# Kernel optimization log

Hardware: AMD Instinct MI355X
Metric: run time of the kernel (lower is better)

The kernel has to match this reference:

```python
import jax, jax.numpy as jnp
import numpy as np

D_MODEL, H, D_FF = 512, 8, 2048
DK = D_MODEL // H
EPS = 1e-5  # torch LayerNorm default


def layer_norm(x, g, b):
    m = jnp.mean(x, axis=-1, keepdims=True)
    v = jnp.mean((x - m) ** 2, axis=-1, keepdims=True)
    return (x - m) * jax.lax.rsqrt(v + EPS) * g + b


def setup_inputs() -> dict:
    key = jax.random.key(0)
    ks = jax.random.split(key, 10)
    B, S = 8, 2048
    s = lambda fan_in: 1.0 / np.sqrt(fan_in)
    return {
        "x": jax.random.normal(ks[0], (B, S, D_MODEL), jnp.float32),
        # per-head projections stacked: [h, d_model, dk] (bias-free Project)
        "wq": jax.random.uniform(ks[1], (H, D_MODEL, DK), jnp.float32, -s(D_MODEL), s(D_MODEL)),
        "wk": jax.random.uniform(ks[2], (H, D_MODEL, DK), jnp.float32, -s(D_MODEL), s(D_MODEL)),
        "wv": jax.random.uniform(ks[3], (H, D_MODEL, DK), jnp.float32, -s(D_MODEL), s(D_MODEL)),
        "wo": jax.random.uniform(ks[4], (D_MODEL, D_MODEL), jnp.float32, -s(D_MODEL), s(D_MODEL)),
        "w1": jax.random.uniform(ks[5], (D_MODEL, D_FF), jnp.float32, -s(D_MODEL), s(D_MODEL)),
        "b1": jax.random.uniform(ks[6], (D_FF,), jnp.float32, -s(D_MODEL), s(D_MODEL)),
        "w2": jax.random.uniform(ks[7], (D_FF, D_MODEL), jnp.float32, -s(D_FF), s(D_FF)),
        "b2": jax.random.uniform(ks[8], (D_MODEL,), jnp.float32, -s(D_FF), s(D_FF)),
        "ln1_g": jnp.ones((D_MODEL,), jnp.float32),
        "ln1_b": jnp.zeros((D_MODEL,), jnp.float32),
        "ln2_g": jnp.ones((D_MODEL,), jnp.float32),
        "ln2_b": jnp.zeros((D_MODEL,), jnp.float32),
    }


def reference(x, wq, wk, wv, wo, w1, b1, w2, b2, ln1_g, ln1_b, ln2_g, ln2_b):
    B, S, D = x.shape
    # --- multi-head self-attention (8 per-head Linears fused into one einsum) ---
    q = jnp.einsum("bsd,hdk->bhsk", x, wq)
    k = jnp.einsum("bsd,hdk->bhsk", x, wk)
    v = jnp.einsum("bsd,hdk->bhsk", x, wv)
    score = jnp.einsum("bhsk,bhtk->bhst", q, k) * (1.0 / np.sqrt(DK))
    attn = jax.nn.softmax(score, axis=-1)
    heads = jnp.einsum("bhst,bhtk->bhsk", attn, v)
    concat = heads.transpose(0, 2, 1, 3).reshape(B, S, D)  # cat over heads
    mha = concat @ wo
    # dropout in eval mode -> identity
    x = layer_norm(mha + x, ln1_g, ln1_b)
    # --- feed-forward ---
    ffn = jax.nn.relu(x @ w1 + b1) @ w2 + b2
    return layer_norm(ffn + x, ln2_g, ln2_b)
```

## Files before the change

### kernel.cpp

```cpp
#include <hip/hip_runtime.h>
#include <hip/hip_bf16.h>
#include <math.h>


#define D_MODEL 512
#define NHEAD   8
#define DKH     64
#define SEQ     2048
#define BATCH   8
#define DFF     2048
#define MROWS   (BATCH * SEQ)
#define QKVLD   1536

typedef __bf16 bf16x8 __attribute__((ext_vector_type(8)));
typedef float  f32x4  __attribute__((ext_vector_type(4)));

__device__ __forceinline__ unsigned short f2bf(float f) {
    union { float f; unsigned u; } v; v.f = f;
    return (unsigned short)((v.u + 0x7FFFu + ((v.u >> 16) & 1u)) >> 16);
}

__device__ __forceinline__ float fexp2(float x) {
    float r; asm("v_exp_f32 %0, %1" : "=v"(r) : "v"(x)); return r;
}

__device__ __forceinline__ f32x4 mfma16(bf16x8 a, bf16x8 b, f32x4 c) {
    return __builtin_amdgcn_mfma_f32_16x16x32_bf16(a, b, c, 0, 0, 0);
}

template<bool BIAS, bool RELU, bool RES, bool OUTF32>
__global__ __launch_bounds__(256)
void mfma_gemm(const unsigned short* __restrict__ Av,
               const unsigned short* __restrict__ Bt,
               const float* __restrict__ bias, const float* __restrict__ res,
               void* __restrict__ Cv, int Kdim, int lda, int ldc)
{
    __shared__ unsigned short As[128][40];
    __shared__ unsigned short Bs[128][40];

    const int tid  = threadIdx.x;
    const int lane = tid & 63;
    const int w    = tid >> 6;
    const int mq   = (w >> 1) << 6;
    const int nq   = (w & 1) << 6;
    const int lrow = lane & 15;
    const int g    = lane >> 4;
    const int lk   = g << 3;

    const int row0 = blockIdx.y << 7;
    const int col0 = blockIdx.x << 7;

    const int sr = tid >> 1;
    const int sk = (tid & 1) << 4;

    uint4 sA0, sA1, sB0, sB1;
    auto loadA = [&](int kt) {
        const unsigned short* ap = Av + (size_t)(row0 + sr) * lda + kt + sk;
        sA0 = *(const uint4*)ap;
        sA1 = *(const uint4*)(ap + 8);
    };
    auto loadB = [&](int kt) {
        const unsigned short* bp = Bt + (size_t)(col0 + sr) * Kdim + kt + sk;
        sB0 = *(const uint4*)bp;
        sB1 = *(const uint4*)(bp + 8);
    };

    const f32x4 zero = {0.f, 0.f, 0.f, 0.f};
    f32x4 acc[4][4];
    #pragma unroll
    for (int i = 0; i < 4; ++i)
        #pragma unroll
        for (int j = 0; j < 4; ++j) acc[i][j] = zero;

    loadA(0); loadB(0);

    for (int kt = 0; kt < Kdim; kt += 32) {
        __syncthreads();
        *(uint4*)&As[sr][sk]     = sA0;
        *(uint4*)&As[sr][sk + 8] = sA1;
        *(uint4*)&Bs[sr][sk]     = sB0;
        *(uint4*)&Bs[sr][sk + 8] = sB1;
        __syncthreads();

        if (kt + 32 < Kdim) { loadA(kt + 32); loadB(kt + 32); }

        bf16x8 af[4], bfv[4];
        #pragma unroll
        for (int mf = 0; mf < 4; ++mf)
            af[mf] = *(const bf16x8*)&As[mq + mf * 16 + lrow][lk];
        #pragma unroll
        for (int nf = 0; nf < 4; ++nf)
            bfv[nf] = *(const bf16x8*)&Bs[nq + nf * 16 + lrow][lk];
        #pragma unroll
        for (int mf = 0; mf < 4; ++mf)
            #pragma unroll
            for (int nf = 0; nf < 4; ++nf)
                acc[mf][nf] = mfma16(af[mf], bfv[nf], acc[mf][nf]);
    }

    const int orow = row0 + mq + g * 4;
    const int ocol = col0 + nq + lrow;
    #pragma unroll
    for (int mf = 0; mf < 4; ++mf) {
        #pragma unroll
        for (int nf = 0; nf < 4; ++nf) {
            const int cc = ocol + nf * 16;
            float bv = 0.f;
            if constexpr (BIAS) bv = bias[cc];
            #pragma unroll
            for (int r = 0; r < 4; ++r) {
                const int rr = orow + mf * 16 + r;
                float v = acc[mf][nf][r];
                if constexpr (BIAS) v += bv;
                if constexpr (RELU) v = fmaxf(v, 0.f);
                if constexpr (RES)  v += res[(size_t)rr * ldc + cc];
                if constexpr (OUTF32) ((float*)Cv)[(size_t)rr * ldc + cc] = v;
                else ((unsigned short*)Cv)[(size_t)rr * ldc + cc] = f2bf(v);
            }
        }
    }
}

__global__ __launch_bounds__(512)
void mfma_attn(unsigned short* __restrict__ qkv)
{
    __shared__ unsigned short Ks[64][72];
    __shared__ unsigned short Vt[64][72];
    __shared__ unsigned short Ps[128][76];

    const int tid  = threadIdx.x;
    const int lane = tid & 63;
    const int w    = tid >> 6;
    const int lrow = lane & 15;
    const int g    = lane >> 4;
    const int lk   = g << 3;

    const int bh = blockIdx.y;
    const int b  = bh >> 3, h = bh & 7;
    const int s0 = blockIdx.x << 7;

    unsigned short* qptr = qkv + ((size_t)(b * SEQ + s0)) * QKVLD + h * DKH;
    const unsigned short* kbase = qkv + ((size_t)(b * SEQ)) * QKVLD + 512 + h * DKH;
    const unsigned short* vbase = qkv + ((size_t)(b * SEQ)) * QKVLD + 1024 + h * DKH;

    bf16x8 qf[2];
    {
        const unsigned short* qp = qptr + (size_t)(w * 16 + lrow) * QKVLD;
        qf[0] = *(const bf16x8*)(qp + lk);
        qf[1] = *(const bf16x8*)(qp + 32 + lk);
    }

    const int kr = tid >> 3, kc = (tid & 7) << 3;
    const int vr = lane,     vc = w << 3;

    uint4 kreg, vreg;
    auto loadKV = [&](int t0) {
        kreg = *(const uint4*)(kbase + (size_t)(t0 + kr) * QKVLD + kc);
        vreg = *(const uint4*)(vbase + (size_t)(t0 + vr) * QKVLD + vc);
    };
    loadKV(0);

    const f32x4 zero = {0.f, 0.f, 0.f, 0.f};
    f32x4 oacc[4];
    float mrun[4], lpart[4];
    #pragma unroll
    for (int i = 0; i < 4; ++i) { oacc[i] = zero; mrun[i] = -INFINITY; lpart[i] = 0.f; }

    for (int t0 = 0; t0 < SEQ; t0 += 64) {
        __syncthreads();
        *(uint4*)&Ks[kr][kc] = kreg;
        {
            const unsigned short* vu = (const unsigned short*)&vreg;
            #pragma unroll
            for (int j = 0; j < 8; ++j) Vt[vc + j][vr] = vu[j];
        }
        __syncthreads();

        if (t0 + 64 < SEQ) loadKV(t0 + 64);

        f32x4 sacc[4];
        #pragma unroll
        for (int nf = 0; nf < 4; ++nf) sacc[nf] = zero;
        __builtin_amdgcn_s_setprio(1);
        #pragma unroll
        for (int kk = 0; kk < 2; ++kk) {
            #pragma unroll
            for (int nf = 0; nf < 4; ++nf) {
                const bf16x8 kf = *(const bf16x8*)&Ks[nf * 16 + lrow][kk * 32 + lk];
                sacc[nf] = mfma16(qf[kk], kf, sacc[nf]);
            }
        }
        __builtin_amdgcn_s_setprio(0);

        float pmax[4];
        bool need = false;
        #pragma unroll
        for (int r = 0; r < 4; ++r) {
            pmax[r] = fmaxf(fmaxf(sacc[0][r], sacc[1][r]),
                            fmaxf(sacc[2][r], sacc[3][r]));
            need |= (pmax[r] > mrun[r] + 8.f);
        }
        if (__any(need)) {
            #pragma unroll
            for (int r = 0; r < 4; ++r) {
                float mt = pmax[r];
                mt = fmaxf(mt, __shfl_xor(mt, 1, 16));
                mt = fmaxf(mt, __shfl_xor(mt, 2, 16));
                mt = fmaxf(mt, __shfl_xor(mt, 4, 16));
                mt = fmaxf(mt, __shfl_xor(mt, 8, 16));
                const float mnew = fmaxf(mrun[r], mt);
                const float alpha = fexp2(mrun[r] - mnew);
                mrun[r] = mnew;
                lpart[r] *= alpha;
                #pragma unroll
                for (int nf = 0; nf < 4; ++nf) oacc[nf][r] *= alpha;
            }
        }
        #pragma unroll
        for (int r = 0; r < 4; ++r) {
            #pragma unroll
            for (int nf = 0; nf < 4; ++nf) {
                const float p = fexp2(sacc[nf][r] - mrun[r]);
                lpart[r] += p;
                Ps[w * 16 + g * 4 + r][nf * 16 + lrow] = f2bf(p);
            }
        }

        __builtin_amdgcn_s_setprio(1);
        #pragma unroll
        for (int kk = 0; kk < 2; ++kk) {
            const bf16x8 pf = *(const bf16x8*)&Ps[w * 16 + lrow][kk * 32 + lk];
            #pragma unroll
            for (int nf = 0; nf < 4; ++nf) {
                const bf16x8 vf = *(const bf16x8*)&Vt[nf * 16 + lrow][kk * 32 + lk];
                oacc[nf] = mfma16(pf, vf, oacc[nf]);
            }
        }
        __builtin_amdgcn_s_setprio(0);
    }

    #pragma unroll
    for (int r = 0; r < 4; ++r) {
        float l = lpart[r];
        l += __shfl_xor(l, 1, 16);
        l += __shfl_xor(l, 2, 16);
        l += __shfl_xor(l, 4, 16);
        l += __shfl_xor(l, 8, 16);
        const float inv = 1.f / l;
        #pragma unroll
        for (int nf = 0; nf < 4; ++nf)
            qptr[(size_t)(w * 16 + g * 4 + r) * QKVLD + nf * 16 + lrow] =
                f2bf(oacc[nf][r] * inv);
    }
}

template<bool WB>
__global__ __launch_bounds__(256)
void ln_kernel(const float* __restrict__ in, const float* __restrict__ gg,
               const float* __restrict__ bb, float* __restrict__ outf,
               unsigned short* __restrict__ outb)
{
    const int row = blockIdx.x * 4 + (threadIdx.x >> 6);
    const int lane = threadIdx.x & 63;
    const float* p = in + (size_t)row * D_MODEL;

    const float4 a = *(const float4*)(p + lane * 4);
    const float4 c = *(const float4*)(p + 256 + lane * 4);
    float sum = a.x + a.y + a.z + a.w + c.x + c.y + c.z + c.w;
    float sq  = a.x*a.x + a.y*a.y + a.z*a.z + a.w*a.w
              + c.x*c.x + c.y*c.y + c.z*c.z + c.w*c.w;
    #pragma unroll
    for (int msk = 1; msk < 64; msk <<= 1) {
        sum += __shfl_xor(sum, msk, 64);
        sq  += __shfl_xor(sq,  msk, 64);
    }
    const float mean = sum * (1.f / 512.f);
    const float var  = sq * (1.f / 512.f) - mean * mean;
    const float rs   = rsqrtf(var + 1e-5f);

    const float4 g0 = *(const float4*)(gg + lane * 4);
    const float4 g1 = *(const float4*)(gg + 256 + lane * 4);
    const float4 b0 = *(const float4*)(bb + lane * 4);
    const float4 b1 = *(const float4*)(bb + 256 + lane * 4);

    float4 o0, o1;
    o0.x = (a.x - mean) * rs * g0.x + b0.x;
    o0.y = (a.y - mean) * rs * g0.y + b0.y;
    o0.z = (a.z - mean) * rs * g0.z + b0.z;
    o0.w = (a.w - mean) * rs * g0.w + b0.w;
    o1.x = (c.x - mean) * rs * g1.x + b1.x;
    o1.y = (c.y - mean) * rs * g1.y + b1.y;
    o1.z = (c.z - mean) * rs * g1.z + b1.z;
    o1.w = (c.w - mean) * rs * g1.w + b1.w;
    *(float4*)(outf + (size_t)row * D_MODEL + lane * 4) = o0;
    *(float4*)(outf + (size_t)row * D_MODEL + 256 + lane * 4) = o1;
    if constexpr (WB) {
        uint2 pa, pb;
        pa.x = f2bf(o0.x) | ((unsigned)f2bf(o0.y) << 16);
        pa.y = f2bf(o0.z) | ((unsigned)f2bf(o0.w) << 16);
        pb.x = f2bf(o1.x) | ((unsigned)f2bf(o1.y) << 16);
        pb.y = f2bf(o1.z) | ((unsigned)f2bf(o1.w) << 16);
        *(uint2*)(outb + (size_t)row * D_MODEL + lane * 4) = pa;
        *(uint2*)(outb + (size_t)row * D_MODEL + 256 + lane * 4) = pb;
    }
}

__global__ __launch_bounds__(256)
void cast_bf16(const float* __restrict__ in, unsigned short* __restrict__ out)
{
    const size_t i = ((size_t)blockIdx.x * 256 + threadIdx.x) * 8;
    const float4 a = *(const float4*)(in + i);
    const float4 b = *(const float4*)(in + i + 4);
    uint4 o;
    o.x = f2bf(a.x) | ((unsigned)f2bf(a.y) << 16);
    o.y = f2bf(a.z) | ((unsigned)f2bf(a.w) << 16);
    o.z = f2bf(b.x) | ((unsigned)f2bf(b.y) << 16);
    o.w = f2bf(b.z) | ((unsigned)f2bf(b.w) << 16);
    *(uint4*)(out + i) = o;
}

__global__ __launch_bounds__(256)
void pack_qkv(const float* __restrict__ wq, const float* __restrict__ wk,
              const float* __restrict__ wv, unsigned short* __restrict__ Wqkv)
{
    const int idx = blockIdx.x * 256 + threadIdx.x;
    const int n = idx >> 9, d = idx & 511;
    const int h = n >> 6, c = n & 63;
    const size_t src = ((size_t)h * 512 + d) * 64 + c;
    Wqkv[idx]                 = f2bf(wq[src] * 0.18033688f);
    Wqkv[idx + 512 * 512]     = f2bf(wk[src]);
    Wqkv[idx + 2 * 512 * 512] = f2bf(wv[src]);
}

__global__ __launch_bounds__(256)
void pack_t(const float* __restrict__ in, unsigned short* __restrict__ out,
            int K, int N)
{
    const int idx = blockIdx.x * 256 + threadIdx.x;
    const int n = idx / K, k = idx % K;
    out[idx] = f2bf(in[(size_t)k * N + n]);
}

extern "C" void kernel_launch(void* const* d_in, const int* in_sizes, int n_in,
                              void* d_out, int out_size, void* d_ws, size_t ws_size,
                              hipStream_t stream)
{
    (void)in_sizes; (void)n_in; (void)out_size;

    const float* x    = (const float*)d_in[0];
    const float* wq   = (const float*)d_in[1];
    const float* wk   = (const float*)d_in[2];
    const float* wv   = (const float*)d_in[3];
    const float* wo   = (const float*)d_in[4];
    const float* w1   = (const float*)d_in[5];
    const float* b1   = (const float*)d_in[6];
    const float* w2   = (const float*)d_in[7];
    const float* b2   = (const float*)d_in[8];
    const float* ln1g = (const float*)d_in[9];
    const float* ln1b = (const float*)d_in[10];
    const float* ln2g = (const float*)d_in[11];
    const float* ln2b = (const float*)d_in[12];
    float* out = (float*)d_out;

    const size_t QKV_BYTES = (size_t)MROWS * QKVLD * 2;
    const size_t Y_BYTES   = (size_t)MROWS * D_MODEL * 4;
    unsigned char* base = (unsigned char*)d_ws;
    unsigned short* qkv  = (unsigned short*)(base);
    float*          y    = (float*)(base + QKV_BYTES);
    unsigned short* Wqkv = (unsigned short*)(base + QKV_BYTES + Y_BYTES);
    unsigned short* wo_t = Wqkv + 3 * 512 * 512;
    unsigned short* w1_t = wo_t + 512 * 512;
    unsigned short* w2_t = w1_t + 2048 * 512;
    unsigned short* hid  = w2_t + 2048 * 512;

    const size_t hid_off = (size_t)((unsigned char*)hid - base);
    const size_t avail = (ws_size > hid_off) ? (ws_size - hid_off) : 0;
    int chunk = (int)(avail / ((size_t)DFF * 2));
    chunk &= ~127;
    if (chunk > MROWS) chunk = MROWS;
    if (chunk < 128)   chunk = 128;

    float* y2 = (float*)qkv;
    unsigned short* xb  = (unsigned short*)d_out;
    unsigned short* x1b = (unsigned short*)d_out;

    pack_qkv<<<1024, 256, 0, stream>>>(wq, wk, wv, Wqkv);
    pack_t<<<(512 * 512) / 256, 256, 0, stream>>>(wo, wo_t, 512, 512);
    pack_t<<<(2048 * 512) / 256, 256, 0, stream>>>(w1, w1_t, 512, 2048);
    pack_t<<<(2048 * 512) / 256, 256, 0, stream>>>(w2, w2_t, 2048, 512);
    cast_bf16<<<(MROWS * D_MODEL) / (256 * 8), 256, 0, stream>>>(x, xb);

    const dim3 blk(256);

    mfma_gemm<false, false, false, false>
        <<<dim3(12, MROWS / 128), blk, 0, stream>>>(xb, Wqkv, nullptr, nullptr,
                                                    qkv, 512, 512, QKVLD);

    mfma_attn<<<dim3(SEQ / 128, BATCH * NHEAD), dim3(512), 0, stream>>>(qkv);

    mfma_gemm<false, false, true, true>
        <<<dim3(4, MROWS / 128), blk, 0, stream>>>(qkv, wo_t, nullptr, x, y,
                                                   512, QKVLD, 512);

    ln_kernel<true><<<MROWS / 4, blk, 0, stream>>>(y, ln1g, ln1b, y, x1b);

    for (int r0 = 0; r0 < MROWS; r0 += chunk) {
        const int rows = (r0 + chunk <= MROWS) ? chunk : (MROWS - r0);
        mfma_gemm<true, true, false, false>
            <<<dim3(DFF / 128, rows / 128), blk, 0, stream>>>(
                x1b + (size_t)r0 * D_MODEL, w1_t, b1, nullptr, hid,
                512, 512, DFF);
        mfma_gemm<true, false, true, true>
            <<<dim3(4, rows / 128), blk, 0, stream>>>(
                hid, w2_t, b2, y + (size_t)r0 * D_MODEL,
                y2 + (size_t)r0 * D_MODEL, DFF, DFF, 512);
    }

    ln_kernel<false><<<MROWS / 4, blk, 0, stream>>>(y2, ln2g, ln2b, out, nullptr);
}
```

Measured before the change: 350.3 us.

## Load GEMM tiles via global_load_lds and use hardware packed bf16 conversion

```diff
diff --git a/kernel.cpp b/kernel.cpp
--- a/kernel.cpp
+++ b/kernel.cpp
@@ -20,12 +20,24 @@
     return (unsigned short)((v.u + 0x7FFFu + ((v.u >> 16) & 1u)) >> 16);
 }
 
+__device__ __forceinline__ unsigned cvtpk(float a, float b) {
+    unsigned r;
+    asm("v_cvt_pk_bf16_f32 %0, %1, %2" : "=v"(r) : "v"(a), "v"(b));
+    return r;
+}
+
 __device__ __forceinline__ float fexp2(float x) {
     float r; asm("v_exp_f32 %0, %1" : "=v"(r) : "v"(x)); return r;
 }
 
 __device__ __forceinline__ f32x4 mfma16(bf16x8 a, bf16x8 b, f32x4 c) {
     return __builtin_amdgcn_mfma_f32_16x16x32_bf16(a, b, c, 0, 0, 0);
+}
+
+__device__ __forceinline__ void gld_lds16(const unsigned short* g, unsigned short* l) {
+    __builtin_amdgcn_global_load_lds(
+        (const __attribute__((address_space(1))) unsigned int*)g,
+        (__attribute__((address_space(3))) unsigned int*)l, 16, 0, 0);
 }
 
 template<bool BIAS, bool RELU, bool RES, bool OUTF32>
@@ -35,8 +47,8 @@
                const float* __restrict__ bias, const float* __restrict__ res,
                void* __restrict__ Cv, int Kdim, int lda, int ldc)
 {
-    __shared__ unsigned short As[128][40];
-    __shared__ unsigned short Bs[128][40];
+    __shared__ unsigned short As[128][32];
+    __shared__ unsigned short Bs[128][32];
 
     const int tid  = threadIdx.x;
     const int lane = tid & 63;
@@ -50,20 +62,9 @@
     const int row0 = blockIdx.y << 7;
     const int col0 = blockIdx.x << 7;
 
-    const int sr = tid >> 1;
-    const int sk = (tid & 1) << 4;
-
-    uint4 sA0, sA1, sB0, sB1;
-    auto loadA = [&](int kt) {
-        const unsigned short* ap = Av + (size_t)(row0 + sr) * lda + kt + sk;
-        sA0 = *(const uint4*)ap;
-        sA1 = *(const uint4*)(ap + 8);
-    };
-    auto loadB = [&](int kt) {
-        const unsigned short* bp = Bt + (size_t)(col0 + sr) * Kdim + kt + sk;
-        sB0 = *(const uint4*)bp;
-        sB1 = *(const uint4*)(bp + 8);
-    };
+    const int c0   = w << 5;
+    const int srow = lane >> 2;
+    const int scol = (lane & 3) << 3;
 
     const f32x4 zero = {0.f, 0.f, 0.f, 0.f};
     f32x4 acc[4][4];
@@ -72,17 +73,13 @@
         #pragma unroll
         for (int j = 0; j < 4; ++j) acc[i][j] = zero;
 
-    loadA(0); loadB(0);
-
     for (int kt = 0; kt < Kdim; kt += 32) {
         __syncthreads();
-        *(uint4*)&As[sr][sk]     = sA0;
-        *(uint4*)&As[sr][sk + 8] = sA1;
-        *(uint4*)&Bs[sr][sk]     = sB0;
-        *(uint4*)&Bs[sr][sk + 8] = sB1;
+        gld_lds16(Av + (size_t)(row0 + c0      + srow) * lda  + kt + scol, &As[c0     ][0]);
+        gld_lds16(Av + (size_t)(row0 + c0 + 16 + srow) * lda  + kt + scol, &As[c0 + 16][0]);
+        gld_lds16(Bt + (size_t)(col0 + c0      + srow) * Kdim + kt + scol, &Bs[c0     ][0]);
+        gld_lds16(Bt + (size_t)(col0 + c0 + 16 + srow) * Kdim + kt + scol, &Bs[c0 + 16][0]);
         __syncthreads();
-
-        if (kt + 32 < Kdim) { loadA(kt + 32); loadB(kt + 32); }
 
         bf16x8 af[4], bfv[4];
         #pragma unroll
@@ -107,15 +104,24 @@
             const int cc = ocol + nf * 16;
             float bv = 0.f;
             if constexpr (BIAS) bv = bias[cc];
+            float v[4];
             #pragma unroll
             for (int r = 0; r < 4; ++r) {
                 const int rr = orow + mf * 16 + r;
-                float v = acc[mf][nf][r];
-                if constexpr (BIAS) v += bv;
-                if constexpr (RELU) v = fmaxf(v, 0.f);
-                if constexpr (RES)  v += res[(size_t)rr * ldc + cc];
-                if constexpr (OUTF32) ((float*)Cv)[(size_t)rr * ldc + cc] = v;
-                else ((unsigned short*)Cv)[(size_t)rr * ldc + cc] = f2bf(v);
+                v[r] = acc[mf][nf][r];
+                if constexpr (BIAS) v[r] += bv;
+                if constexpr (RELU) v[r] = fmaxf(v[r], 0.f);
+                if constexpr (RES)  v[r] += res[(size_t)rr * ldc + cc];
+                if constexpr (OUTF32) ((float*)Cv)[(size_t)rr * ldc + cc] = v[r];
+            }
+            if constexpr (!OUTF32) {
+                const unsigned u01 = cvtpk(v[0], v[1]);
+                const unsigned u23 = cvtpk(v[2], v[3]);
+                unsigned short* cp = (unsigned short*)Cv + (size_t)(orow + mf * 16) * ldc + cc;
+                cp[0]                 = (unsigned short)u01;
+                cp[(size_t)ldc]       = (unsigned short)(u01 >> 16);
+                cp[(size_t)ldc * 2]   = (unsigned short)u23;
+                cp[(size_t)ldc * 3]   = (unsigned short)(u23 >> 16);
             }
         }
     }
@@ -218,12 +224,18 @@
         }
         #pragma unroll
         for (int r = 0; r < 4; ++r) {
-            #pragma unroll
-            for (int nf = 0; nf < 4; ++nf) {
-                const float p = fexp2(sacc[nf][r] - mrun[r]);
-                lpart[r] += p;
-                Ps[w * 16 + g * 4 + r][nf * 16 + lrow] = f2bf(p);
-            }
+            const float p0 = fexp2(sacc[0][r] - mrun[r]);
+            const float p1 = fexp2(sacc[1][r] - mrun[r]);
+            const float p2 = fexp2(sacc[2][r] - mrun[r]);
+            const float p3 = fexp2(sacc[3][r] - mrun[r]);
+            lpart[r] += (p0 + p1) + (p2 + p3);
+            const unsigned u01 = cvtpk(p0, p1);
+            const unsigned u23 = cvtpk(p2, p3);
+            unsigned short* prow = &Ps[w * 16 + g * 4 + r][lrow];
+            prow[0]  = (unsigned short)u01;
+            prow[16] = (unsigned short)(u01 >> 16);
+            prow[32] = (unsigned short)u23;
+            prow[48] = (unsigned short)(u23 >> 16);
         }
 
         __builtin_amdgcn_s_setprio(1);
@@ -296,10 +308,10 @@
     *(float4*)(outf + (size_t)row * D_MODEL + 256 + lane * 4) = o1;
     if constexpr (WB) {
         uint2 pa, pb;
-        pa.x = f2bf(o0.x) | ((unsigned)f2bf(o0.y) << 16);
-        pa.y = f2bf(o0.z) | ((unsigned)f2bf(o0.w) << 16);
-        pb.x = f2bf(o1.x) | ((unsigned)f2bf(o1.y) << 16);
-        pb.y = f2bf(o1.z) | ((unsigned)f2bf(o1.w) << 16);
+        pa.x = cvtpk(o0.x, o0.y);
+        pa.y = cvtpk(o0.z, o0.w);
+        pb.x = cvtpk(o1.x, o1.y);
+        pb.y = cvtpk(o1.z, o1.w);
         *(uint2*)(outb + (size_t)row * D_MODEL + lane * 4) = pa;
         *(uint2*)(outb + (size_t)row * D_MODEL + 256 + lane * 4) = pb;
     }
@@ -312,10 +324,10 @@
     const float4 a = *(const float4*)(in + i);
     const float4 b = *(const float4*)(in + i + 4);
     uint4 o;
-    o.x = f2bf(a.x) | ((unsigned)f2bf(a.y) << 16);
-    o.y = f2bf(a.z) | ((unsigned)f2bf(a.w) << 16);
-    o.z = f2bf(b.x) | ((unsigned)f2bf(b.y) << 16);
-    o.w = f2bf(b.z) | ((unsigned)f2bf(b.w) << 16);
+    o.x = cvtpk(a.x, a.y);
+    o.y = cvtpk(a.z, a.w);
+    o.z = cvtpk(b.x, b.y);
+    o.w = cvtpk(b.z, b.w);
     *(uint4*)(out + i) = o;
 }
 
```

Result: slower. 360.7 us (+3.0%).
